# Kernel tuning notes

Hardware: AMD Instinct MI355X
Metric: run time of the kernel (lower is better)

## Reference

```python
import jax, jax.numpy as jnp
import numpy as np

B, N, E, DIN, DOUT = 4, 10000, 320000, 128, 128
EPS = 1e-5


def setup_inputs() -> dict:
    key = jax.random.key(0)
    ks = jax.random.split(key, 10)
    x = jax.random.normal(ks[0], (B, N, DIN), dtype=jnp.float32)
    edge_index = jax.random.randint(ks[1], (2, E), 0, N, dtype=jnp.int64)
    norm = jax.random.uniform(ks[2], (E, 1), dtype=jnp.float32)
    W_w = jax.random.normal(ks[3], (DOUT, DIN), dtype=jnp.float32) / np.sqrt(DIN)
    W_b = jax.random.normal(ks[4], (DOUT,), dtype=jnp.float32) * 0.01
    bn_gamma = jnp.ones((N,), dtype=jnp.float32)
    bn_beta = jnp.zeros((N,), dtype=jnp.float32)
    bn_mean = jax.random.normal(ks[5], (N,), dtype=jnp.float32) * 0.01
    bn_var = jax.random.uniform(ks[6], (N,), dtype=jnp.float32, minval=0.5, maxval=1.5)
    return {"x": x, "edge_index": edge_index, "norm": norm, "W_w": W_w,
            "W_b": W_b, "bn_gamma": bn_gamma, "bn_beta": bn_beta,
            "bn_mean": bn_mean, "bn_var": bn_var}


def reference(x, edge_index, norm, W_w, W_b, bn_gamma, bn_beta, bn_mean, bn_var):
    # Dropout is identity in eval mode.
    h = jnp.einsum('bnf,of->bno', x, W_w) + W_b            # [B, N, DOUT]
    # BatchNorm1d over channel dim = node dim (eval mode, running stats)
    inv = jax.lax.rsqrt(bn_var + EPS)
    h = (h - bn_mean[None, :, None]) * (inv * bn_gamma)[None, :, None] + bn_beta[None, :, None]
    h = jax.nn.gelu(h, approximate=False)                  # torch GELU default = exact erf
    # gather -> scale -> scatter-add message passing
    msgs = h[:, edge_index[1], :] * norm                   # [B, E, DOUT]
    out = jnp.zeros_like(h).at[:, edge_index[0], :].add(msgs)
    return out
```

## Files before the change

### kernel.cpp

```cpp
#include <hip/hip_runtime.h>
#include <math.h>

#define DIN 128
#define DOUT 128
#define EPS 1e-5f
#define CHUNK_SHIFT 11
#define CAPC 32

typedef unsigned short ushort_t;
typedef __bf16 bf16x8 __attribute__((ext_vector_type(8)));
typedef float f32x16 __attribute__((ext_vector_type(16)));

__device__ __forceinline__ unsigned int f2bf_u(float f) {
    union { float f; unsigned int i; } v; v.f = f;
    unsigned int x = v.i;
    unsigned int r = x + 0x7fffu + ((x >> 16) & 1u);
    return r >> 16;
}
__device__ __forceinline__ ushort_t f2bf(float f) { return (ushort_t)f2bf_u(f); }

__global__ __launch_bounds__(256) void prep_kernel(
    const float* __restrict__ W, uint4* __restrict__ wb,
    int* __restrict__ counts, int total_counts)
{
    int t = blockIdx.x * blockDim.x + threadIdx.x;
    if (t < 2048) {
        int ct = t >> 9, kc = (t >> 6) & 7, l = t & 63;
        int o = ct * 32 + (l & 31);
        int f = kc * 16 + ((l >> 5) << 3);
        const float4* src = (const float4*)(W + o * 128 + f);
        float4 v0 = src[0], v1 = src[1];
        uint4 pk;
        pk.x = f2bf_u(v0.x) | (f2bf_u(v0.y) << 16);
        pk.y = f2bf_u(v0.z) | (f2bf_u(v0.w) << 16);
        pk.z = f2bf_u(v1.x) | (f2bf_u(v1.y) << 16);
        pk.w = f2bf_u(v1.z) | (f2bf_u(v1.w) << 16);
        wb[t] = pk;
    }
    for (int i = t; i < total_counts; i += gridDim.x * blockDim.x) counts[i] = 0;
}

__global__ __launch_bounds__(256, 4) void gemm_bn_gelu_fill(
    const float* __restrict__ x, const uint4* __restrict__ wb,
    const float* __restrict__ bias, const float* __restrict__ gamma,
    const float* __restrict__ beta, const float* __restrict__ mean,
    const float* __restrict__ var, ushort_t* __restrict__ hb,
    const int* __restrict__ ei, const float* __restrict__ norm,
    int* __restrict__ counts, unsigned int* __restrict__ csr,
    int N, int E, int nc)
{
    __shared__ ushort_t XH[8192];
    __shared__ float sm_mu[16], sm_sc[16], sm_bt[16];

    const int tid = threadIdx.x;
    const int n0 = blockIdx.x * 16;
    const int w = tid >> 6;
    const int lane = tid & 63;

    bf16x8 bfr[8];
#pragma unroll
    for (int kc = 0; kc < 8; ++kc)
        bfr[kc] = *(const bf16x8*)(wb + (w * 512 + kc * 64 + lane));

    {
        const int gid = blockIdx.x * blockDim.x + tid;
        const int stride = gridDim.x * blockDim.x;
        for (int e = gid; e < E; e += 2 * stride) {
            int ep = e + stride;
            int has2 = ep < E;
            int dst0 = ei[e];
            int src0 = ei[E + e];
            float nm0 = norm[e];
            int dst1 = 0, src1 = 0;
            float nm1 = 0.f;
            if (has2) { dst1 = ei[ep]; src1 = ei[E + ep]; nm1 = norm[ep]; }
            int b0 = dst0 * nc + (src0 >> CHUNK_SHIFT);
            int slot0 = atomicAdd(&counts[b0], 1);
            if (slot0 < CAPC)
                csr[((size_t)b0 << 5) + slot0] =
                    ((unsigned int)src0 << 16) | f2bf_u(nm0);
            if (has2) {
                int b1 = dst1 * nc + (src1 >> CHUNK_SHIFT);
                int slot1 = atomicAdd(&counts[b1], 1);
                if (slot1 < CAPC)
                    csr[((size_t)b1 << 5) + slot1] =
                        ((unsigned int)src1 << 16) | f2bf_u(nm1);
            }
        }
    }

    if (tid < 16) {
        int n = n0 + tid;
        sm_mu[tid] = mean[n];
        sm_sc[tid] = rsqrtf(var[n] + EPS) * gamma[n];
        sm_bt[tid] = beta[n];
    }

#pragma unroll
    for (int it = 0; it < 4; ++it) {
        int tup = tid + it * 256;
        int rt = tup >> 9, kc = (tup >> 6) & 7, l = tup & 63;
        int r = rt * 32 + (l & 31);
        int b = r >> 4, i = r & 15;
        size_t grow = (size_t)b * N + n0 + i;
        int f = kc * 16 + ((l >> 5) << 3);
        const float4* src = (const float4*)(x + grow * 128 + f);
        float4 v0 = src[0], v1 = src[1];
        uint4 pk;
        pk.x = f2bf_u(v0.x) | (f2bf_u(v0.y) << 16);
        pk.y = f2bf_u(v0.z) | (f2bf_u(v0.w) << 16);
        pk.z = f2bf_u(v1.x) | (f2bf_u(v1.y) << 16);
        pk.w = f2bf_u(v1.z) | (f2bf_u(v1.w) << 16);
        *(uint4*)&XH[tup * 8] = pk;
    }
    __syncthreads();

    f32x16 acc0 = {};
    f32x16 acc1 = {};
#pragma unroll
    for (int kc = 0; kc < 8; ++kc) {
        bf16x8 a0 = *(const bf16x8*)&XH[(kc * 64 + lane) * 8];
        bf16x8 a1 = *(const bf16x8*)&XH[(512 * 8) + (kc * 64 + lane) * 8];
        acc0 = __builtin_amdgcn_mfma_f32_32x32x16_bf16(a0, bfr[kc], acc0, 0, 0, 0);
        acc1 = __builtin_amdgcn_mfma_f32_32x32x16_bf16(a1, bfr[kc], acc1, 0, 0, 0);
    }
    __syncthreads();

    const int col = w * 32 + (lane & 31);
    const float bias_c = bias[col];
    const int hi4 = (lane >> 5) * 4;
#pragma unroll
    for (int reg = 0; reg < 8; ++reg) {
        int i0 = (reg & 3) + 8 * (reg >> 2) + hi4;
        float mu = sm_mu[i0], sc = sm_sc[i0], bt = sm_bt[i0];
        float vals[4] = { acc0[reg], acc0[reg + 8], acc1[reg], acc1[reg + 8] };
        ushort4 pk;
        {
            float v = vals[0] + bias_c; v = (v - mu) * sc + bt;
            pk.x = f2bf(0.5f * v * (1.0f + erff(v * 0.70710678118654752f)));
        }
        {
            float v = vals[1] + bias_c; v = (v - mu) * sc + bt;
            pk.y = f2bf(0.5f * v * (1.0f + erff(v * 0.70710678118654752f)));
        }
        {
            float v = vals[2] + bias_c; v = (v - mu) * sc + bt;
            pk.z = f2bf(0.5f * v * (1.0f + erff(v * 0.70710678118654752f)));
        }
        {
            float v = vals[3] + bias_c; v = (v - mu) * sc + bt;
            pk.w = f2bf(0.5f * v * (1.0f + erff(v * 0.70710678118654752f)));
        }
        *(ushort4*)&XH[((i0 << 7) + col) << 2] = pk;
    }
    __syncthreads();

    {
        const float4* s = (const float4*)XH;
        float4* d = (float4*)(hb + (size_t)n0 * 512);
#pragma unroll
        for (int i = tid; i < 1024; i += 256) d[i] = s[i];
    }
}

__device__ __forceinline__ void fma8(float* acc, int4 h, float wgt) {
    union { unsigned int i; float f; } t;
    unsigned int u;
    u = (unsigned int)h.x;
    t.i = u << 16;          acc[0] = fmaf(t.f, wgt, acc[0]);
    t.i = u & 0xffff0000u;  acc[1] = fmaf(t.f, wgt, acc[1]);
    u = (unsigned int)h.y;
    t.i = u << 16;          acc[2] = fmaf(t.f, wgt, acc[2]);
    t.i = u & 0xffff0000u;  acc[3] = fmaf(t.f, wgt, acc[3]);
    u = (unsigned int)h.z;
    t.i = u << 16;          acc[4] = fmaf(t.f, wgt, acc[4]);
    t.i = u & 0xffff0000u;  acc[5] = fmaf(t.f, wgt, acc[5]);
    u = (unsigned int)h.w;
    t.i = u << 16;          acc[6] = fmaf(t.f, wgt, acc[6]);
    t.i = u & 0xffff0000u;  acc[7] = fmaf(t.f, wgt, acc[7]);
}

__global__ __launch_bounds__(256) void gather_kernel(
    const ushort_t* __restrict__ hb, const int* __restrict__ counts,
    const unsigned int* __restrict__ csr, float* __restrict__ out,
    int N, int nc)
{
    const int w = threadIdx.x >> 6;
    const int lane = threadIdx.x & 63;
    const int n = blockIdx.x * 4 + w;
    if (n >= N) return;

    float acc[8] = {};
    const int l2 = lane & (CAPC - 1);

    for (int c = 0; c < nc; ++c) {
        int cnt = counts[n * nc + c];
        if (cnt > CAPC) cnt = CAPC;
        if (cnt == 0) continue;
        const unsigned int* bucket = csr + ((size_t)(n * nc + c) << 5);
        unsigned int meta = bucket[l2];
        for (int j = 0; j < cnt; j += 8) {
            unsigned int m[8];
#pragma unroll
            for (int k = 0; k < 8; ++k) {
                unsigned int mk =
                    (unsigned int)__builtin_amdgcn_readlane((int)meta, j + k);
                m[k] = (j + k < cnt) ? mk : 0u;
            }
            int4 h0 = *(const int4*)(hb + (size_t)(m[0] >> 16) * 512 + lane * 8);
            int4 h1 = *(const int4*)(hb + (size_t)(m[1] >> 16) * 512 + lane * 8);
            int4 h2 = *(const int4*)(hb + (size_t)(m[2] >> 16) * 512 + lane * 8);
            int4 h3 = *(const int4*)(hb + (size_t)(m[3] >> 16) * 512 + lane * 8);
            int4 h4 = *(const int4*)(hb + (size_t)(m[4] >> 16) * 512 + lane * 8);
            int4 h5 = *(const int4*)(hb + (size_t)(m[5] >> 16) * 512 + lane * 8);
            int4 h6 = *(const int4*)(hb + (size_t)(m[6] >> 16) * 512 + lane * 8);
            int4 h7 = *(const int4*)(hb + (size_t)(m[7] >> 16) * 512 + lane * 8);
            union { unsigned int i; float f; } wv;
            wv.i = m[0] << 16; fma8(acc, h0, wv.f);
            wv.i = m[1] << 16; fma8(acc, h1, wv.f);
            wv.i = m[2] << 16; fma8(acc, h2, wv.f);
            wv.i = m[3] << 16; fma8(acc, h3, wv.f);
            wv.i = m[4] << 16; fma8(acc, h4, wv.f);
            wv.i = m[5] << 16; fma8(acc, h5, wv.f);
            wv.i = m[6] << 16; fma8(acc, h6, wv.f);
            wv.i = m[7] << 16; fma8(acc, h7, wv.f);
        }
    }

    const size_t bstride = (size_t)N * DOUT;
    float* op = out + (size_t)n * DOUT + lane * 2;
#pragma unroll
    for (int b = 0; b < 4; ++b) {
        float2 v; v.x = acc[b]; v.y = acc[4 + b];
        *(float2*)(op + b * bstride) = v;
    }
}

extern "C" void kernel_launch(void* const* d_in, const int* in_sizes, int n_in,
                              void* d_out, int out_size, void* d_ws, size_t ws_size,
                              hipStream_t stream)
{
    const float* x     = (const float*)d_in[0];
    const int*   ei    = (const int*)d_in[1];
    const float* norm  = (const float*)d_in[2];
    const float* W_w   = (const float*)d_in[3];
    const float* W_b   = (const float*)d_in[4];
    const float* gamma = (const float*)d_in[5];
    const float* beta  = (const float*)d_in[6];
    const float* mean  = (const float*)d_in[7];
    const float* var   = (const float*)d_in[8];
    float* out = (float*)d_out;

    const int N = in_sizes[5];
    const int E = in_sizes[2];
    const int nc = (N + (1 << CHUNK_SHIFT) - 1) >> CHUNK_SHIFT;

    ushort_t* hb      = (ushort_t*)d_ws;
    uint4* wb         = (uint4*)(hb + (size_t)N * 512);
    int* counts       = (int*)(wb + 2048);
    unsigned int* csr = (unsigned int*)(counts + (size_t)N * nc);

    int prep_blocks = (N * nc + 255) / 256;
    prep_kernel<<<prep_blocks, 256, 0, stream>>>(W_w, wb, counts, N * nc);

    int gemm_blocks = N / 16;
    gemm_bn_gelu_fill<<<gemm_blocks, 256, 0, stream>>>(
        x, wb, W_b, gamma, beta, mean, var, hb, ei, norm, counts, csr, N, E, nc);

    gather_kernel<<<(N + 3) / 4, 256, 0, stream>>>(hb, counts, csr, out, N, nc);
}
```

Baseline: 144.8 us.

## Use polynomial erf for GELU and process two nodes per gather wavefront

Replaces the library erff in the fused GEMM/BN/GELU epilogue with an Abramowitz-Stegun polynomial that uses hardware rcp and exp2, cutting per-element transcendental cost at a small accuracy loss. The gather kernel now gives each wavefront two destination nodes, loading both nodes' counts and bucket metadata up front to expose more independent memory traffic. It also adds a launch-bounds occupancy hint and halves the grid. Doubling accumulators raises register pressure, and the two nodes are still processed one after the other.

```diff
diff --git a/kernel.cpp b/kernel.cpp
--- a/kernel.cpp
+++ b/kernel.cpp
@@ -18,6 +18,19 @@
     return r >> 16;
 }
 __device__ __forceinline__ ushort_t f2bf(float f) { return (ushort_t)f2bf_u(f); }
+
+__device__ __forceinline__ float gelu_exact(float v) {
+    float ax = fabsf(v) * 0.70710678118654752f;
+    float t  = __builtin_amdgcn_rcpf(fmaf(0.3275911f, ax, 1.0f));
+    float p  = fmaf(fmaf(fmaf(fmaf(1.061405429f, t, -1.453152027f),
+                              t, 1.421413741f),
+                         t, -0.284496736f),
+                    t, 0.254829592f) * t;
+    float e  = __builtin_amdgcn_exp2f(ax * ax * -1.4426950408889634f);
+    float erf_ax = fmaf(-p, e, 1.0f);
+    float erfv = (v < 0.0f) ? -erf_ax : erf_ax;
+    return 0.5f * v * (1.0f + erfv);
+}
 
 __global__ __launch_bounds__(256) void prep_kernel(
     const float* __restrict__ W, uint4* __restrict__ wb,
@@ -135,22 +148,10 @@
         float mu = sm_mu[i0], sc = sm_sc[i0], bt = sm_bt[i0];
         float vals[4] = { acc0[reg], acc0[reg + 8], acc1[reg], acc1[reg + 8] };
         ushort4 pk;
-        {
-            float v = vals[0] + bias_c; v = (v - mu) * sc + bt;
-            pk.x = f2bf(0.5f * v * (1.0f + erff(v * 0.70710678118654752f)));
-        }
-        {
-            float v = vals[1] + bias_c; v = (v - mu) * sc + bt;
-            pk.y = f2bf(0.5f * v * (1.0f + erff(v * 0.70710678118654752f)));
-        }
-        {
-            float v = vals[2] + bias_c; v = (v - mu) * sc + bt;
-            pk.z = f2bf(0.5f * v * (1.0f + erff(v * 0.70710678118654752f)));
-        }
-        {
-            float v = vals[3] + bias_c; v = (v - mu) * sc + bt;
-            pk.w = f2bf(0.5f * v * (1.0f + erff(v * 0.70710678118654752f)));
-        }
+        { float v = (vals[0] + bias_c - mu) * sc + bt; pk.x = f2bf(gelu_exact(v)); }
+        { float v = (vals[1] + bias_c - mu) * sc + bt; pk.y = f2bf(gelu_exact(v)); }
+        { float v = (vals[2] + bias_c - mu) * sc + bt; pk.z = f2bf(gelu_exact(v)); }
+        { float v = (vals[3] + bias_c - mu) * sc + bt; pk.w = f2bf(gelu_exact(v)); }
         *(ushort4*)&XH[((i0 << 7) + col) << 2] = pk;
     }
     __syncthreads();
@@ -180,59 +181,78 @@
     t.i = u & 0xffff0000u;  acc[7] = fmaf(t.f, wgt, acc[7]);
 }
 
-__global__ __launch_bounds__(256) void gather_kernel(
+__device__ __forceinline__ void burst8(const ushort_t* __restrict__ hb,
+                                       unsigned int meta, int j, int cnt,
+                                       int lane, float* acc)
+{
+    unsigned int m[8];
+#pragma unroll
+    for (int k = 0; k < 8; ++k) {
+        unsigned int mk =
+            (unsigned int)__builtin_amdgcn_readlane((int)meta, j + k);
+        m[k] = (j + k < cnt) ? mk : 0u;
+    }
+    int4 h0 = *(const int4*)(hb + (size_t)(m[0] >> 16) * 512 + lane * 8);
+    int4 h1 = *(const int4*)(hb + (size_t)(m[1] >> 16) * 512 + lane * 8);
+    int4 h2 = *(const int4*)(hb + (size_t)(m[2] >> 16) * 512 + lane * 8);
+    int4 h3 = *(const int4*)(hb + (size_t)(m[3] >> 16) * 512 + lane * 8);
+    int4 h4 = *(const int4*)(hb + (size_t)(m[4] >> 16) * 512 + lane * 8);
+    int4 h5 = *(const int4*)(hb + (size_t)(m[5] >> 16) * 512 + lane * 8);
+    int4 h6 = *(const int4*)(hb + (size_t)(m[6] >> 16) * 512 + lane * 8);
+    int4 h7 = *(const int4*)(hb + (size_t)(m[7] >> 16) * 512 + lane * 8);
+    union { unsigned int i; float f; } wv;
+    wv.i = m[0] << 16; fma8(acc, h0, wv.f);
+    wv.i = m[1] << 16; fma8(acc, h1, wv.f);
+    wv.i = m[2] << 16; fma8(acc, h2, wv.f);
+    wv.i = m[3] << 16; fma8(acc, h3, wv.f);
+    wv.i = m[4] << 16; fma8(acc, h4, wv.f);
+    wv.i = m[5] << 16; fma8(acc, h5, wv.f);
+    wv.i = m[6] << 16; fma8(acc, h6, wv.f);
+    wv.i = m[7] << 16; fma8(acc, h7, wv.f);
+}
+
+__global__ __launch_bounds__(256, 5) void gather_kernel(
     const ushort_t* __restrict__ hb, const int* __restrict__ counts,
     const unsigned int* __restrict__ csr, float* __restrict__ out,
     int N, int nc)
 {
     const int w = threadIdx.x >> 6;
     const int lane = threadIdx.x & 63;
-    const int n = blockIdx.x * 4 + w;
-    if (n >= N) return;
-
-    float acc[8] = {};
+    const int na = blockIdx.x * 8 + w * 2;
+    if (na >= N) return;
+    const int nb = na + 1;
+    const bool hasB = (nb < N);
+
+    float accA[8] = {}, accB[8] = {};
     const int l2 = lane & (CAPC - 1);
 
     for (int c = 0; c < nc; ++c) {
-        int cnt = counts[n * nc + c];
-        if (cnt > CAPC) cnt = CAPC;
-        if (cnt == 0) continue;
-        const unsigned int* bucket = csr + ((size_t)(n * nc + c) << 5);
-        unsigned int meta = bucket[l2];
-        for (int j = 0; j < cnt; j += 8) {
-            unsigned int m[8];
-#pragma unroll
-            for (int k = 0; k < 8; ++k) {
-                unsigned int mk =
-                    (unsigned int)__builtin_amdgcn_readlane((int)meta, j + k);
-                m[k] = (j + k < cnt) ? mk : 0u;
-            }
-            int4 h0 = *(const int4*)(hb + (size_t)(m[0] >> 16) * 512 + lane * 8);
-            int4 h1 = *(const int4*)(hb + (size_t)(m[1] >> 16) * 512 + lane * 8);
-            int4 h2 = *(const int4*)(hb + (size_t)(m[2] >> 16) * 512 + lane * 8);
-            int4 h3 = *(const int4*)(hb + (size_t)(m[3] >> 16) * 512 + lane * 8);
-            int4 h4 = *(const int4*)(hb + (size_t)(m[4] >> 16) * 512 + lane * 8);
-            int4 h5 = *(const int4*)(hb + (size_t)(m[5] >> 16) * 512 + lane * 8);
-            int4 h6 = *(const int4*)(hb + (size_t)(m[6] >> 16) * 512 + lane * 8);
-            int4 h7 = *(const int4*)(hb + (size_t)(m[7] >> 16) * 512 + lane * 8);
-            union { unsigned int i; float f; } wv;
-            wv.i = m[0] << 16; fma8(acc, h0, wv.f);
-            wv.i = m[1] << 16; fma8(acc, h1, wv.f);
-            wv.i = m[2] << 16; fma8(acc, h2, wv.f);
-            wv.i = m[3] << 16; fma8(acc, h3, wv.f);
-            wv.i = m[4] << 16; fma8(acc, h4, wv.f);
-            wv.i = m[5] << 16; fma8(acc, h5, wv.f);
-            wv.i = m[6] << 16; fma8(acc, h6, wv.f);
-            wv.i = m[7] << 16; fma8(acc, h7, wv.f);
+        const int ia = na * nc + c;
+        const int ib = ia + nc;
+        int cntA = counts[ia];
+        int cntB = hasB ? counts[ib] : 0;
+        unsigned int metaA = csr[((size_t)ia << 5) + l2];
+        unsigned int metaB = hasB ? csr[((size_t)ib << 5) + l2] : 0u;
+        if (cntA > CAPC) cntA = CAPC;
+        if (cntB > CAPC) cntB = CAPC;
+        for (int j = 0; j < cntA; j += 8) burst8(hb, metaA, j, cntA, lane, accA);
+        for (int j = 0; j < cntB; j += 8) burst8(hb, metaB, j, cntB, lane, accB);
+    }
+
+    const size_t bstride = (size_t)N * DOUT;
+    float* opA = out + (size_t)na * DOUT + lane * 2;
+#pragma unroll
+    for (int b = 0; b < 4; ++b) {
+        float2 v; v.x = accA[b]; v.y = accA[4 + b];
+        *(float2*)(opA + b * bstride) = v;
+    }
+    if (hasB) {
+        float* opB = out + (size_t)nb * DOUT + lane * 2;
+#pragma unroll
+        for (int b = 0; b < 4; ++b) {
+            float2 v; v.x = accB[b]; v.y = accB[4 + b];
+            *(float2*)(opB + b * bstride) = v;
         }
-    }
-
-    const size_t bstride = (size_t)N * DOUT;
-    float* op = out + (size_t)n * DOUT + lane * 2;
-#pragma unroll
-    for (int b = 0; b < 4; ++b) {
-        float2 v; v.x = acc[b]; v.y = acc[4 + b];
-        *(float2*)(op + b * bstride) = v;
     }
 }
 
@@ -267,5 +287,5 @@
     gemm_bn_gelu_fill<<<gemm_blocks, 256, 0, stream>>>(
         x, wb, W_b, gamma, beta, mean, var, hb, ei, norm, counts, csr, N, E, nc);
 
-    gather_kernel<<<(N + 3) / 4, 256, 0, stream>>>(hb, counts, csr, out, N, nc);
-}
+    gather_kernel<<<(N + 7) / 8, 256, 0, stream>>>(hb, counts, csr, out, N, nc);
+}
```

Result: faster. 140.0 us (-3.3%).
